# Performance work log

Hardware: AMD Instinct MI355X
Metric: run time of the kernel (lower is better)

## Reference

```python
import jax, jax.numpy as jnp
import numpy as np

# DAG configuration (fixed, mirrors the networkx dG used at construction time)
B = 4096          # batch
N_INP = 4096      # genes
L0 = 512          # leaf GO terms, each mapped to G disjoint genes
G = 8             # genes per leaf term
H = 16            # module_neurons (uniform per-module hidden size)
FAN = 8           # children per internal module -> input size FAN*H = 128
L1, L2 = 64, 8    # internal level sizes; root has L2=8 children


def setup_inputs() -> dict:
    key = jax.random.key(0)
    ks = jax.random.split(key, 8)
    s = lambda *sh: 0.1
    x = jax.random.normal(ks[0], (B, N_INP), dtype=jnp.float32)
    # Gene (RestrictedLayer) effective weights: kernel*connections is one-hot,
    # so only kernel[gene_idx[m,j], j] survives -> store as [L0, G] + bias.
    Wg = jax.random.normal(ks[1], (L0, G), dtype=jnp.float32) * 0.1
    bg = jax.random.normal(ks[2], (L0, G), dtype=jnp.float32) * 0.1
    # Per-level module Dense kernels (sigmoid, no bias)
    W0 = jax.random.normal(ks[3], (L0, G, H), dtype=jnp.float32) * 0.1       # leaf terms: G -> H
    W1 = jax.random.normal(ks[4], (L1, FAN * H, H), dtype=jnp.float32) * 0.1  # 128 -> 16
    W2 = jax.random.normal(ks[5], (L2, FAN * H, H), dtype=jnp.float32) * 0.1  # 128 -> 16
    W3 = jax.random.normal(ks[6], (FAN * H, H), dtype=jnp.float32) * 0.1      # root: 128 -> 16
    Wf = jax.random.normal(ks[7], (H, 1), dtype=jnp.float32) * 0.1            # final linear, no bias
    return {"x": x, "Wg": Wg, "bg": bg, "W0": W0, "W1": W1, "W2": W2,
            "W3": W3, "Wf": Wf}


def reference(x, Wg, bg, W0, W1, W2, W3, Wf):
    b = x.shape[0]
    # Input gene layers (RestrictedLayer, linear activation):
    # leaf m owns contiguous genes [m*G, (m+1)*G) -> gather is a reshape.
    gene_out = x.reshape(b, L0, G) * Wg + bg                    # [B, L0, G]
    # Level 0 (leaf GO terms): Dense(G->H), sigmoid, no bias
    h0 = jax.nn.sigmoid(jnp.einsum('bmg,mgh->bmh', gene_out, W0))   # [B, L0, H]
    # Level 1: concat FAN children's H outputs -> Dense(FAN*H -> H), sigmoid
    h1 = jax.nn.sigmoid(jnp.einsum('bmk,mkh->bmh',
                                   h0.reshape(b, L1, FAN * H), W1))  # [B, L1, H]
    # Level 2
    h2 = jax.nn.sigmoid(jnp.einsum('bmk,mkh->bmh',
                                   h1.reshape(b, L2, FAN * H), W2))  # [B, L2, H]
    # Root 'GO:output'
    hr = jax.nn.sigmoid(h2.reshape(b, FAN * H) @ W3)                 # [B, H]
    # Final Dense(1), linear, no bias
    return hr @ Wf                                                   # [B, 1]
```

## Files before the change

kernel.cpp:

```cpp
#include <hip/hip_runtime.h>
#include <hip/hip_bf16.h>


#define TB 16
#define XSS 520
#define H0S 1032
#define H1S 136

typedef __attribute__((ext_vector_type(8))) short short8;
typedef __attribute__((ext_vector_type(4))) float floatx4;

__device__ __forceinline__ float sigf(float v) {
    return __builtin_amdgcn_rcpf(1.0f + __expf(-v));
}
__device__ __forceinline__ float bflo(unsigned int p) {
    return __builtin_bit_cast(float, p << 16);
}
__device__ __forceinline__ float bfhi(unsigned int p) {
    return __builtin_bit_cast(float, p & 0xffff0000u);
}
__device__ __forceinline__ unsigned int f2bf_u32(float f) {
    unsigned int u = __builtin_bit_cast(unsigned int, f);
    return (u + 0x7fffu + ((u >> 16) & 1u)) >> 16;
}
__device__ __forceinline__ unsigned short f2bf(float f) {
    return (unsigned short)f2bf_u32(f);
}
__device__ __forceinline__ unsigned int f2bf2(float lo, float hi) {
    return f2bf_u32(lo) | (f2bf_u32(hi) << 16);
}

__global__ __launch_bounds__(256) void k_prep(
    const float* __restrict__ W1, const float* __restrict__ W2,
    unsigned short* __restrict__ W1t, unsigned short* __restrict__ W2t)
{
    __shared__ float wl[128 * 17];
    const int mb = blockIdx.x;
    const float* src = (mb < 64) ? (W1 + (size_t)mb * 2048)
                                 : (W2 + (size_t)(mb - 64) * 2048);
    unsigned short* dst = (mb < 64) ? (W1t + (size_t)mb * 2048)
                                    : (W2t + (size_t)(mb - 64) * 2048);
    const int tid = threadIdx.x;
#pragma unroll
    for (int i = 0; i < 8; ++i) {
        const int idx = tid + i * 256;
        wl[(idx >> 4) * 17 + (idx & 15)] = src[idx];
    }
    __syncthreads();
#pragma unroll
    for (int i = 0; i < 4; ++i) {
        const int u  = tid + i * 256;
        const int h  = u >> 6;
        const int k  = (u & 63) * 2;
        ((unsigned int*)dst)[u] = f2bf2(wl[k * 17 + h], wl[(k + 1) * 17 + h]);
    }
}

__global__ __launch_bounds__(256) void k_tree(
    const float* __restrict__ x, const float* __restrict__ Wg,
    const float* __restrict__ bg, const float* __restrict__ W0,
    const unsigned short* __restrict__ W1t, const unsigned short* __restrict__ W2t,
    float* __restrict__ h2ws)
{
    __shared__ __align__(16) unsigned short xs[TB * XSS];
    __shared__ __align__(16) unsigned short h0s[TB * H0S];
    unsigned short* h1u = xs;

    const int tid  = threadIdx.x;
    const int s    = blockIdx.x & 7;
    const int b0   = (blockIdx.x >> 3) * TB;
    const int lane = tid & 63;
    const int wv   = tid >> 6;

    const float* xbase = x + (size_t)b0 * 4096 + s * 512;
    uint2 xp[8];
#pragma unroll
    for (int t = 0; t < 8; ++t) {
        const int i = tid + t * 256;
        const int r = i >> 7, c4 = i & 127;
        const float4 v = *(const float4*)(xbase + (size_t)r * 4096 + c4 * 4);
        xp[t] = make_uint2(f2bf2(v.x, v.y), f2bf2(v.z, v.w));
    }

    const int m_l = tid >> 2;
    const int hq  = tid & 3;
    const int m   = s * 64 + m_l;
    float4 w0r[8];
#pragma unroll
    for (int g = 0; g < 8; ++g)
        w0r[g] = *(const float4*)(W0 + (size_t)m * 128 + g * 16 + hq * 4);
    const float4 wg0 = *(const float4*)(Wg + m * 8);
    const float4 wg1 = *(const float4*)(Wg + m * 8 + 4);
    const float4 bg0 = *(const float4*)(bg + m * 8);
    const float4 bg1 = *(const float4*)(bg + m * 8 + 4);

    const int n = lane & 15, q = lane >> 4;
    short8 w1r[2][4];
#pragma unroll
    for (int jj = 0; jj < 2; ++jj) {
        const unsigned short* w1m =
            W1t + ((size_t)(s * 8 + wv * 2 + jj) * 16 + n) * 128 + q * 8;
#pragma unroll
        for (int ks = 0; ks < 4; ++ks)
            w1r[jj][ks] = *(const short8*)(w1m + ks * 32);
    }
    short8 w2r[4];
    if (wv == 0) {
        const unsigned short* w2m = W2t + ((size_t)s * 16 + n) * 128 + q * 8;
#pragma unroll
        for (int ks = 0; ks < 4; ++ks) w2r[ks] = *(const short8*)(w2m + ks * 32);
    }

#pragma unroll
    for (int t = 0; t < 8; ++t) {
        const int i = tid + t * 256;
        const int r = i >> 7, c4 = i & 127;
        *(uint2*)&xs[r * XSS + c4 * 4] = xp[t];
    }
    __syncthreads();

    {
        unsigned short* h0base = &h0s[m_l * 16 + hq * 4];
#pragma unroll 4
        for (int b = 0; b < TB; ++b) {
            const uint4 xv = *(const uint4*)&xs[b * XSS + m_l * 8];
            float gene[8];
            gene[0] = fmaf(bflo(xv.x), wg0.x, bg0.x);
            gene[1] = fmaf(bfhi(xv.x), wg0.y, bg0.y);
            gene[2] = fmaf(bflo(xv.y), wg0.z, bg0.z);
            gene[3] = fmaf(bfhi(xv.y), wg0.w, bg0.w);
            gene[4] = fmaf(bflo(xv.z), wg1.x, bg1.x);
            gene[5] = fmaf(bfhi(xv.z), wg1.y, bg1.y);
            gene[6] = fmaf(bflo(xv.w), wg1.z, bg1.z);
            gene[7] = fmaf(bfhi(xv.w), wg1.w, bg1.w);
            float a0 = 0.f, a1 = 0.f, a2 = 0.f, a3 = 0.f;
#pragma unroll
            for (int g = 0; g < 8; ++g) {
                a0 = fmaf(gene[g], w0r[g].x, a0);
                a1 = fmaf(gene[g], w0r[g].y, a1);
                a2 = fmaf(gene[g], w0r[g].z, a2);
                a3 = fmaf(gene[g], w0r[g].w, a3);
            }
            *(uint2*)(h0base + b * H0S) =
                make_uint2(f2bf2(sigf(a0), sigf(a1)), f2bf2(sigf(a2), sigf(a3)));
        }
    }
    __syncthreads();

    {
#pragma unroll
        for (int jj = 0; jj < 2; ++jj) {
            const int j = wv * 2 + jj;
            const unsigned short* am = &h0s[n * H0S + j * 128 + q * 8];
            floatx4 acc = {0.f, 0.f, 0.f, 0.f};
#pragma unroll
            for (int ks = 0; ks < 4; ++ks) {
                const short8 av = *(const short8*)(am + ks * 32);
                acc = __builtin_amdgcn_mfma_f32_16x16x32_bf16(av, w1r[jj][ks], acc, 0, 0, 0);
            }
#pragma unroll
            for (int r = 0; r < 4; ++r)
                h1u[(q * 4 + r) * H1S + j * 16 + n] = f2bf(sigf(acc[r]));
        }
    }
    __syncthreads();

    if (wv == 0) {
        const unsigned short* am = &h1u[n * H1S + q * 8];
        floatx4 acc = {0.f, 0.f, 0.f, 0.f};
#pragma unroll
        for (int ks = 0; ks < 4; ++ks) {
            const short8 av = *(const short8*)(am + ks * 32);
            acc = __builtin_amdgcn_mfma_f32_16x16x32_bf16(av, w2r[ks], acc, 0, 0, 0);
        }
#pragma unroll
        for (int r = 0; r < 4; ++r)
            h2ws[(size_t)(b0 + q * 4 + r) * 128 + s * 16 + n] = sigf(acc[r]);
    }
}

__global__ __launch_bounds__(128) void k_root(
    const float* __restrict__ h2ws, const float* __restrict__ W3,
    const float* __restrict__ Wf, float* __restrict__ out)
{
    __shared__ float w3s[2048];
    __shared__ float wfs[16];
    const int tid = threadIdx.x;
#pragma unroll
    for (int t = 0; t < 16; ++t) w3s[tid + t * 128] = W3[tid + t * 128];
    if (tid < 16) wfs[tid] = Wf[tid];
    __syncthreads();

    const int h = tid & 15;
    const int b = blockIdx.x * 8 + (tid >> 4);
    const float4* hp = (const float4*)(h2ws + (size_t)b * 128);
    float acc = 0.f;
#pragma unroll
    for (int k4 = 0; k4 < 32; ++k4) {
        const float4 hv = hp[k4];
        acc = fmaf(hv.x, w3s[(k4 * 4 + 0) * 16 + h], acc);
        acc = fmaf(hv.y, w3s[(k4 * 4 + 1) * 16 + h], acc);
        acc = fmaf(hv.z, w3s[(k4 * 4 + 2) * 16 + h], acc);
        acc = fmaf(hv.w, w3s[(k4 * 4 + 3) * 16 + h], acc);
    }
    float v = sigf(acc) * wfs[h];
    v += __shfl_down(v, 8, 16);
    v += __shfl_down(v, 4, 16);
    v += __shfl_down(v, 2, 16);
    v += __shfl_down(v, 1, 16);
    if (h == 0) out[b] = v;
}

extern "C" void kernel_launch(void* const* d_in, const int* in_sizes, int n_in,
                              void* d_out, int out_size, void* d_ws, size_t ws_size,
                              hipStream_t stream) {
    const float* x  = (const float*)d_in[0];
    const float* Wg = (const float*)d_in[1];
    const float* bg = (const float*)d_in[2];
    const float* W0 = (const float*)d_in[3];
    const float* W1 = (const float*)d_in[4];
    const float* W2 = (const float*)d_in[5];
    const float* W3 = (const float*)d_in[6];
    const float* Wf = (const float*)d_in[7];
    float* out = (float*)d_out;

    float* h2 = (float*)d_ws;
    unsigned short* W1t = (unsigned short*)((char*)d_ws + (size_t)2 * 1024 * 1024);
    unsigned short* W2t = W1t + (size_t)64 * 2048;

    k_prep<<<dim3(72), dim3(256), 0, stream>>>(W1, W2, W1t, W2t);
    k_tree<<<dim3((4096 / TB) * 8), dim3(256), 0, stream>>>(x, Wg, bg, W0, W1t, W2t, h2);
    k_root<<<dim3(4096 / 8), dim3(128), 0, stream>>>(h2, W3, Wf, out);
}
```

Measured before the change: 121.9 us.

## Fold gene layer into W0 and compute leaf level with MFMA

Precomputes Wg*W0 as bf16 MFMA fragments and folds bg into a per-leaf bias in the prep kernel, so the leaf-level Dense runs as block-diagonal 16x16x32 bf16 MFMAs instead of scalar FMAs. The padded shared-memory strides are replaced with XOR-swizzled layouts to avoid bank conflicts, and the root kernel is widened to 256 threads with vectorised W3 staging. It also sets a launch-bounds occupancy hint. Risks are extra prep work and bf16 rounding of the folded weights.

```diff
diff --git a/kernel.cpp b/kernel.cpp
--- a/kernel.cpp
+++ b/kernel.cpp
@@ -3,8 +3,6 @@
 
 
 #define TB 16
-#define XSS 520
-#define H0S 1032
 #define H1S 136
 
 typedef __attribute__((ext_vector_type(8))) short short8;
@@ -12,12 +10,6 @@
 
 __device__ __forceinline__ float sigf(float v) {
     return __builtin_amdgcn_rcpf(1.0f + __expf(-v));
-}
-__device__ __forceinline__ float bflo(unsigned int p) {
-    return __builtin_bit_cast(float, p << 16);
-}
-__device__ __forceinline__ float bfhi(unsigned int p) {
-    return __builtin_bit_cast(float, p & 0xffff0000u);
 }
 __device__ __forceinline__ unsigned int f2bf_u32(float f) {
     unsigned int u = __builtin_bit_cast(unsigned int, f);
@@ -32,38 +24,99 @@
 
 __global__ __launch_bounds__(256) void k_prep(
     const float* __restrict__ W1, const float* __restrict__ W2,
-    unsigned short* __restrict__ W1t, unsigned short* __restrict__ W2t)
+    const float* __restrict__ Wg, const float* __restrict__ bg,
+    const float* __restrict__ W0,
+    unsigned short* __restrict__ W1t, unsigned short* __restrict__ W2t,
+    unsigned short* __restrict__ W0f, float* __restrict__ bias0g)
 {
     __shared__ float wl[128 * 17];
-    const int mb = blockIdx.x;
-    const float* src = (mb < 64) ? (W1 + (size_t)mb * 2048)
-                                 : (W2 + (size_t)(mb - 64) * 2048);
-    unsigned short* dst = (mb < 64) ? (W1t + (size_t)mb * 2048)
-                                    : (W2t + (size_t)(mb - 64) * 2048);
+    const int mb  = blockIdx.x;
     const int tid = threadIdx.x;
-#pragma unroll
-    for (int i = 0; i < 8; ++i) {
-        const int idx = tid + i * 256;
-        wl[(idx >> 4) * 17 + (idx & 15)] = src[idx];
-    }
-    __syncthreads();
+    if (mb < 72) {
+        const float* src = (mb < 64) ? (W1 + (size_t)mb * 2048)
+                                     : (W2 + (size_t)(mb - 64) * 2048);
+        unsigned short* dst = (mb < 64) ? (W1t + (size_t)mb * 2048)
+                                        : (W2t + (size_t)(mb - 64) * 2048);
+#pragma unroll
+        for (int i = 0; i < 8; ++i) {
+            const int idx = tid + i * 256;
+            wl[(idx >> 4) * 17 + (idx & 15)] = src[idx];
+        }
+        __syncthreads();
+#pragma unroll
+        for (int i = 0; i < 4; ++i) {
+            const int u  = tid + i * 256;
+            const int h  = u >> 6;
+            const int k  = (u & 63) * 2;
+            ((unsigned int*)dst)[u] = f2bf2(wl[k * 17 + h], wl[(k + 1) * 17 + h]);
+        }
+    } else {
+        const int idx = mb - 72;
+        const int sub = tid >> 6, l = tid & 63;
+#pragma unroll
+        for (int it = 0; it < 2; ++it) {
+            const int m = idx * 8 + it * 4 + sub;
+            uint4 v = make_uint4(0u, 0u, 0u, 0u);
+            if (l < 16) {
+                float p[8];
+                float bsum = 0.f;
+#pragma unroll
+                for (int j = 0; j < 8; ++j) {
+                    const float w = W0[(size_t)m * 128 + j * 16 + l];
+                    p[j] = Wg[m * 8 + j] * w;
+                    bsum = fmaf(bg[m * 8 + j], w, bsum);
+                }
+                v.x = f2bf2(p[0], p[1]);
+                v.y = f2bf2(p[2], p[3]);
+                v.z = f2bf2(p[4], p[5]);
+                v.w = f2bf2(p[6], p[7]);
+                bias0g[m * 16 + l] = bsum;
+            }
+            *(uint4*)(W0f + (size_t)m * 512 + l * 8) = v;
+        }
+    }
+}
+
+struct FragG { uint4 a0, a1, a2, a3; float4 b0, b1, b2, b3; };
+
+__device__ __forceinline__ void load4(FragG& f, const unsigned short* w0fp,
+                                      const float* bp, int g) {
+    f.a0 = *(const uint4*)(w0fp + (size_t)(g * 4 + 0) * 512);
+    f.a1 = *(const uint4*)(w0fp + (size_t)(g * 4 + 1) * 512);
+    f.a2 = *(const uint4*)(w0fp + (size_t)(g * 4 + 2) * 512);
+    f.a3 = *(const uint4*)(w0fp + (size_t)(g * 4 + 3) * 512);
+    f.b0 = *(const float4*)(bp + (g * 4 + 0) * 16);
+    f.b1 = *(const float4*)(bp + (g * 4 + 1) * 16);
+    f.b2 = *(const float4*)(bp + (g * 4 + 2) * 16);
+    f.b3 = *(const float4*)(bp + (g * 4 + 3) * 16);
+}
+
+__device__ __forceinline__ void comp4(const FragG& f, int g, int m0,
+                                      const char* xrd, char* h0wr,
+                                      int brow, int q) {
 #pragma unroll
     for (int i = 0; i < 4; ++i) {
-        const int u  = tid + i * 256;
-        const int h  = u >> 6;
-        const int k  = (u & 63) * 2;
-        ((unsigned int*)dst)[u] = f2bf2(wl[k * 17 + h], wl[(k + 1) * 17 + h]);
-    }
-}
-
-__global__ __launch_bounds__(256) void k_tree(
-    const float* __restrict__ x, const float* __restrict__ Wg,
-    const float* __restrict__ bg, const float* __restrict__ W0,
+        const uint4  a4 = (i == 0) ? f.a0 : (i == 1) ? f.a1 : (i == 2) ? f.a2 : f.a3;
+        const float4 b4 = (i == 0) ? f.b0 : (i == 1) ? f.b1 : (i == 2) ? f.b2 : f.b3;
+        const int mloc = m0 + g * 4 + i;
+        const short8 bv = *(const short8*)(xrd + ((mloc * 16) ^ ((brow & 7) << 4)));
+        floatx4 acc = {b4.x, b4.y, b4.z, b4.w};
+        acc = __builtin_amdgcn_mfma_f32_16x16x32_bf16(
+                  __builtin_bit_cast(short8, a4), bv, acc, 0, 0, 0);
+        *(uint2*)(h0wr + ((mloc * 32 + q * 8) ^ ((brow & 7) << 4))) =
+            make_uint2(f2bf2(sigf(acc[0]), sigf(acc[1])),
+                       f2bf2(sigf(acc[2]), sigf(acc[3])));
+    }
+}
+
+__global__ __launch_bounds__(256, 3) void k_tree(
+    const float* __restrict__ x,
+    const unsigned short* __restrict__ W0f, const float* __restrict__ bias0g,
     const unsigned short* __restrict__ W1t, const unsigned short* __restrict__ W2t,
     float* __restrict__ h2ws)
 {
-    __shared__ __align__(16) unsigned short xs[TB * XSS];
-    __shared__ __align__(16) unsigned short h0s[TB * H0S];
+    __shared__ __align__(16) unsigned short xs[16 * 512];
+    __shared__ __align__(16) unsigned short h0s[16 * 1024];
     unsigned short* h1u = xs;
 
     const int tid  = threadIdx.x;
@@ -71,6 +124,7 @@
     const int b0   = (blockIdx.x >> 3) * TB;
     const int lane = tid & 63;
     const int wv   = tid >> 6;
+    const int n    = lane & 15, q = lane >> 4;
 
     const float* xbase = x + (size_t)b0 * 4096 + s * 512;
     uint2 xp[8];
@@ -82,19 +136,6 @@
         xp[t] = make_uint2(f2bf2(v.x, v.y), f2bf2(v.z, v.w));
     }
 
-    const int m_l = tid >> 2;
-    const int hq  = tid & 3;
-    const int m   = s * 64 + m_l;
-    float4 w0r[8];
-#pragma unroll
-    for (int g = 0; g < 8; ++g)
-        w0r[g] = *(const float4*)(W0 + (size_t)m * 128 + g * 16 + hq * 4);
-    const float4 wg0 = *(const float4*)(Wg + m * 8);
-    const float4 wg1 = *(const float4*)(Wg + m * 8 + 4);
-    const float4 bg0 = *(const float4*)(bg + m * 8);
-    const float4 bg1 = *(const float4*)(bg + m * 8 + 4);
-
-    const int n = lane & 15, q = lane >> 4;
     short8 w1r[2][4];
 #pragma unroll
     for (int jj = 0; jj < 2; ++jj) {
@@ -115,47 +156,40 @@
     for (int t = 0; t < 8; ++t) {
         const int i = tid + t * 256;
         const int r = i >> 7, c4 = i & 127;
-        *(uint2*)&xs[r * XSS + c4 * 4] = xp[t];
+        *(uint2*)((char*)xs + r * 1024 + ((c4 * 8) ^ ((r & 7) << 4))) = xp[t];
     }
     __syncthreads();
 
     {
-        unsigned short* h0base = &h0s[m_l * 16 + hq * 4];
-#pragma unroll 4
-        for (int b = 0; b < TB; ++b) {
-            const uint4 xv = *(const uint4*)&xs[b * XSS + m_l * 8];
-            float gene[8];
-            gene[0] = fmaf(bflo(xv.x), wg0.x, bg0.x);
-            gene[1] = fmaf(bfhi(xv.x), wg0.y, bg0.y);
-            gene[2] = fmaf(bflo(xv.y), wg0.z, bg0.z);
-            gene[3] = fmaf(bfhi(xv.y), wg0.w, bg0.w);
-            gene[4] = fmaf(bflo(xv.z), wg1.x, bg1.x);
-            gene[5] = fmaf(bfhi(xv.z), wg1.y, bg1.y);
-            gene[6] = fmaf(bflo(xv.w), wg1.z, bg1.z);
-            gene[7] = fmaf(bfhi(xv.w), wg1.w, bg1.w);
-            float a0 = 0.f, a1 = 0.f, a2 = 0.f, a3 = 0.f;
-#pragma unroll
-            for (int g = 0; g < 8; ++g) {
-                a0 = fmaf(gene[g], w0r[g].x, a0);
-                a1 = fmaf(gene[g], w0r[g].y, a1);
-                a2 = fmaf(gene[g], w0r[g].z, a2);
-                a3 = fmaf(gene[g], w0r[g].w, a3);
-            }
-            *(uint2*)(h0base + b * H0S) =
-                make_uint2(f2bf2(sigf(a0), sigf(a1)), f2bf2(sigf(a2), sigf(a3)));
-        }
+        const int m0 = wv * 16;
+        const unsigned short* w0fp = W0f + ((size_t)(s * 64 + m0) * 64 + lane) * 8;
+        const float* bp = bias0g + (size_t)(s * 64 + m0) * 16 + q * 4;
+        const int brow = lane & 15;
+        const char* xrd = (const char*)xs + brow * 1024;
+        char* h0wr = (char*)h0s + brow * 2048;
+        FragG fA, fB;
+        load4(fA, w0fp, bp, 0);
+        load4(fB, w0fp, bp, 1);
+        comp4(fA, 0, m0, xrd, h0wr, brow, q);
+        load4(fA, w0fp, bp, 2);
+        comp4(fB, 1, m0, xrd, h0wr, brow, q);
+        load4(fB, w0fp, bp, 3);
+        comp4(fA, 2, m0, xrd, h0wr, brow, q);
+        comp4(fB, 3, m0, xrd, h0wr, brow, q);
     }
     __syncthreads();
 
     {
+        char* const h0b = (char*)h0s;
+        const int swn = (n & 7) << 4;
 #pragma unroll
         for (int jj = 0; jj < 2; ++jj) {
             const int j = wv * 2 + jj;
-            const unsigned short* am = &h0s[n * H0S + j * 128 + q * 8];
             floatx4 acc = {0.f, 0.f, 0.f, 0.f};
 #pragma unroll
             for (int ks = 0; ks < 4; ++ks) {
-                const short8 av = *(const short8*)(am + ks * 32);
+                const short8 av = *(const short8*)(h0b + n * 2048 +
+                                   ((j * 256 + q * 16 + ks * 64) ^ swn));
                 acc = __builtin_amdgcn_mfma_f32_16x16x32_bf16(av, w1r[jj][ks], acc, 0, 0, 0);
             }
 #pragma unroll
@@ -179,20 +213,20 @@
     }
 }
 
-__global__ __launch_bounds__(128) void k_root(
+__global__ __launch_bounds__(256) void k_root(
     const float* __restrict__ h2ws, const float* __restrict__ W3,
     const float* __restrict__ Wf, float* __restrict__ out)
 {
     __shared__ float w3s[2048];
     __shared__ float wfs[16];
     const int tid = threadIdx.x;
-#pragma unroll
-    for (int t = 0; t < 16; ++t) w3s[tid + t * 128] = W3[tid + t * 128];
+    *(float4*)&w3s[tid * 8]     = *(const float4*)(W3 + tid * 8);
+    *(float4*)&w3s[tid * 8 + 4] = *(const float4*)(W3 + tid * 8 + 4);
     if (tid < 16) wfs[tid] = Wf[tid];
     __syncthreads();
 
     const int h = tid & 15;
-    const int b = blockIdx.x * 8 + (tid >> 4);
+    const int b = blockIdx.x * 16 + (tid >> 4);
     const float4* hp = (const float4*)(h2ws + (size_t)b * 128);
     float acc = 0.f;
 #pragma unroll
@@ -227,8 +261,13 @@
     float* h2 = (float*)d_ws;
     unsigned short* W1t = (unsigned short*)((char*)d_ws + (size_t)2 * 1024 * 1024);
     unsigned short* W2t = W1t + (size_t)64 * 2048;
-
-    k_prep<<<dim3(72), dim3(256), 0, stream>>>(W1, W2, W1t, W2t);
-    k_tree<<<dim3((4096 / TB) * 8), dim3(256), 0, stream>>>(x, Wg, bg, W0, W1t, W2t, h2);
-    k_root<<<dim3(4096 / 8), dim3(128), 0, stream>>>(h2, W3, Wf, out);
-}
+    unsigned short* W0f = (unsigned short*)((char*)d_ws + (size_t)2 * 1024 * 1024
+                                                        + (size_t)512 * 1024);
+    float* bias0g = (float*)((char*)d_ws + (size_t)3 * 1024 * 1024);
+
+    k_prep<<<dim3(136), dim3(256), 0, stream>>>(W1, W2, Wg, bg, W0,
+                                                W1t, W2t, W0f, bias0g);
+    k_tree<<<dim3((4096 / TB) * 8), dim3(256), 0, stream>>>(
+        x, W0f, bias0g, W1t, W2t, h2);
+    k_root<<<dim3(4096 / 16), dim3(256), 0, stream>>>(h2, W3, Wf, out);
+}
```

Measured after the change: 118.8 us. -2.5%, faster.
